# Kernel optimization log

Measured on AMD Instinct MI355X. Metric: run time of the kernel, lower is better.

## Reference

```python
import jax, jax.numpy as jnp
import numpy as np

D, H, FFN_D, B, LT, LS = 1024, 16, 4096, 4, 1024, 1024
EPS = 1e-5  # torch LayerNorm default
NEG = -10000000000.0


def setup_inputs() -> dict:
    key = jax.random.key(0)
    ks = iter(jax.random.split(key, 64))
    s = 0.02
    n = lambda shape: jax.random.normal(next(ks), shape, jnp.float32) * s
    inp = {
        'enc_output': n((LS, B, D)),
        'embedded': n((LT, B, D)),
        'src_mask': jnp.zeros((LS, B), jnp.bool_),
        'tgt_mask': jnp.zeros((LT, B), jnp.bool_),
    }
    for p in ('mmha', 'ed'):
        for w in ('q', 'k', 'v', 'o'):
            inp[f'{p}_w{w}'] = n((D, D))
            inp[f'{p}_b{w}'] = jnp.zeros((D,), jnp.float32)
    inp['ffn_w1'] = n((FFN_D, D)); inp['ffn_b1'] = jnp.zeros((FFN_D,), jnp.float32)
    inp['ffn_w2'] = n((D, FFN_D)); inp['ffn_b2'] = jnp.zeros((D,), jnp.float32)
    for i in range(3):
        inp[f'ln{i}_g'] = jnp.ones((D,), jnp.float32)
        inp[f'ln{i}_b'] = jnp.zeros((D,), jnp.float32)
    return inp


def _ln(x, g, b):
    m = x.mean(-1, keepdims=True)
    v = ((x - m) ** 2).mean(-1, keepdims=True)
    return (x - m) / jnp.sqrt(v + EPS) * g + b


def _mha(qx, kx, vx, wq, bq, wk, bk, wv, bv, wo, bo, mask):
    # qx: (Lq,B,D); kx,vx: (Lk,B,D); mask broadcastable to (B,H,Lq,Lk), True=masked
    Lq, Bn, Dm = qx.shape
    dk = Dm // H
    proj = lambda x, w, bb: (x @ w.T + bb).reshape(x.shape[0], Bn, H, dk).transpose(1, 2, 0, 3)
    q, k, v = proj(qx, wq, bq), proj(kx, wk, bk), proj(vx, wv, bv)  # (B,H,L,dk)
    scores = jnp.einsum('bhqd,bhkd->bhqk', q, k) / np.float32(np.sqrt(dk))
    scores = jnp.where(mask, NEG, scores)  # masked_fill semantics
    w = jax.nn.softmax(scores, axis=-1)  # dropout is identity in eval
    attn = jnp.einsum('bhqk,bhkd->bhqd', w, v).transpose(2, 0, 1, 3).reshape(Lq, Bn, Dm)
    return attn @ wo.T + bo


def reference(enc_output, embedded, src_mask, tgt_mask,
              mmha_wq, mmha_bq, mmha_wk, mmha_bk, mmha_wv, mmha_bv, mmha_wo, mmha_bo,
              ed_wq, ed_bq, ed_wk, ed_bk, ed_wv, ed_bv, ed_wo, ed_bo,
              ffn_w1, ffn_b1, ffn_w2, ffn_b2,
              ln0_g, ln0_b, ln1_g, ln1_b, ln2_g, ln2_b):
    Lt = embedded.shape[0]
    causal = jnp.triu(jnp.ones((Lt, Lt), jnp.bool_), 1)[None, None]      # (1,1,Lt,Lt)
    tmask = tgt_mask.T[:, None, None, :]                                  # (B,1,1,Lt)
    # Sublayer 0: masked self-attention (computed but UNUSED downstream,
    # faithfully mirroring the original forward which discards self_attn).
    self_attn = embedded + _mha(_ln(embedded, ln0_g, ln0_b), _ln(embedded, ln0_g, ln0_b), _ln(embedded, ln0_g, ln0_b),
                                mmha_wq, mmha_bq, mmha_wk, mmha_bk, mmha_wv, mmha_bv, mmha_wo, mmha_bo,
                                causal | tmask)
    del self_attn
    # Sublayer 1: enc-dec attention; residual input is `embedded` (as in source).
    smask = src_mask.T[:, None, None, :]                                  # (B,1,1,Ls)
    q_in = _ln(embedded, ln1_g, ln1_b)
    enc_dec = embedded + _mha(q_in, enc_output, enc_output,
                              ed_wq, ed_bq, ed_wk, ed_bk, ed_wv, ed_bv, ed_wo, ed_bo,
                              smask)
    # Sublayer 2: FFN
    z = _ln(enc_dec, ln2_g, ln2_b)
    ffn = jnp.maximum(z @ ffn_w1.T + ffn_b1, 0.0) @ ffn_w2.T + ffn_b2
    return enc_dec + ffn
```

## Files before the change

### kernel.cpp

```cpp
#include <hip/hip_runtime.h>
#include <cstdint>
#include <math.h>

constexpr int NH  = 16;
constexpr int DKH = 64;
constexpr int SEQ = 1024;
constexpr int NB  = 4;
constexpr int DM  = 1024;
constexpr int DF  = 4096;

typedef __bf16 bf16;
typedef __bf16 bf16x4 __attribute__((ext_vector_type(4)));
typedef __bf16 bf16x8 __attribute__((ext_vector_type(8)));
typedef float  f32x4  __attribute__((ext_vector_type(4)));

#define MFMA16(a, b, c) __builtin_amdgcn_mfma_f32_16x16x32_bf16((a), (b), (c), 0, 0, 0)

__device__ __forceinline__ void gload_lds16(const void* g, void* l) {
  __builtin_amdgcn_global_load_lds(
      (const __attribute__((address_space(1))) unsigned int*)(uintptr_t)g,
      (__attribute__((address_space(3))) unsigned int*)(uintptr_t)l,
      16, 0, 0);
}

template <int BK>
__device__ __forceinline__ int swz(int row) {
  return (BK == 32) ? ((row >> 1) & 3) : (row & 7);
}

template <int ROWS, int BK>
__device__ __forceinline__ void stage_tile(const bf16* __restrict__ g, int ldg,
                                           bf16* __restrict__ l, int t) {
  constexpr int ITER = ROWS * BK / 2048;
#pragma unroll
  for (int i = 0; i < ITER; ++i) {
    const int off = (i * 256 + t) * 8;
    const int row = off / BK;
    const int cc = (off & (BK - 1)) >> 3;
    const int sc = cc ^ swz<BK>(row);
    gload_lds16(&g[(size_t)row * ldg + (sc << 3)], &l[off]);
  }
}

__global__ __launch_bounds__(256) void cast4_kernel(const float* __restrict__ i0, const float* __restrict__ i1,
                                                    const float* __restrict__ i2, const float* __restrict__ i3,
                                                    bf16* __restrict__ o0, bf16* __restrict__ o1,
                                                    bf16* __restrict__ o2, bf16* __restrict__ o3) {
  const int sel = blockIdx.x >> 10;
  const int idx = (blockIdx.x & 1023) * 256 + threadIdx.x;
  const float* in = sel == 0 ? i0 : sel == 1 ? i1 : sel == 2 ? i2 : i3;
  bf16* out = sel == 0 ? o0 : sel == 1 ? o1 : sel == 2 ? o2 : o3;
  const float4 v = ((const float4*)in)[idx];
  bf16x4 ov;
  ov[0] = (bf16)v.x; ov[1] = (bf16)v.y; ov[2] = (bf16)v.z; ov[3] = (bf16)v.w;
  ((bf16x4*)out)[idx] = ov;
}

__global__ __launch_bounds__(256) void cast3_kernel(const float* __restrict__ i0, const float* __restrict__ i1,
                                                    const float* __restrict__ i2,
                                                    bf16* __restrict__ o0, bf16* __restrict__ o1,
                                                    bf16* __restrict__ o2) {
  const int sel = blockIdx.x >> 12;
  const int idx = (blockIdx.x & 4095) * 256 + threadIdx.x;
  const float* in = sel == 0 ? i0 : sel == 1 ? i1 : i2;
  bf16* out = sel == 0 ? o0 : sel == 1 ? o1 : o2;
  const float4 v = ((const float4*)in)[idx];
  bf16x4 ov;
  ov[0] = (bf16)v.x; ov[1] = (bf16)v.y; ov[2] = (bf16)v.z; ov[3] = (bf16)v.w;
  ((bf16x4*)out)[idx] = ov;
}

__global__ __launch_bounds__(256) void ln_kernel(const float* __restrict__ x,
                                                 const float* __restrict__ gam,
                                                 const float* __restrict__ bet,
                                                 bf16* __restrict__ out) {
  const int row = blockIdx.x, t = threadIdx.x;
  const float4 v = ((const float4*)(x + (size_t)row * DM))[t];
  float s  = v.x + v.y + v.z + v.w;
  float s2 = v.x * v.x + v.y * v.y + v.z * v.z + v.w * v.w;
#pragma unroll
  for (int m = 1; m < 64; m <<= 1) { s += __shfl_xor(s, m); s2 += __shfl_xor(s2, m); }
  __shared__ float red[8];
  const int w = t >> 6;
  if ((t & 63) == 0) { red[w] = s; red[4 + w] = s2; }
  __syncthreads();
  s  = red[0] + red[1] + red[2] + red[3];
  s2 = red[4] + red[5] + red[6] + red[7];
  const float mean = s * (1.f / DM);
  const float var  = s2 * (1.f / DM) - mean * mean;
  const float rstd = rsqrtf(var + 1e-5f);
  const float4 g4 = ((const float4*)gam)[t];
  const float4 b4 = ((const float4*)bet)[t];
  bf16x4 ov;
  ov[0] = (bf16)((v.x - mean) * rstd * g4.x + b4.x);
  ov[1] = (bf16)((v.y - mean) * rstd * g4.y + b4.y);
  ov[2] = (bf16)((v.z - mean) * rstd * g4.z + b4.z);
  ov[3] = (bf16)((v.w - mean) * rstd * g4.w + b4.w);
  ((bf16x4*)(out + (size_t)row * DM))[t] = ov;
}

enum { EPI_QKV = 0, EPI_O = 3, EPI_F1 = 4, EPI_F2 = 5 };

struct GParams {
  const bf16* A;
  const bf16* A2;
  const bf16* W;
  const float* b0;
  const float* b1;
  const float* b2;
  const float* resid;
  void* out;
  void* out1;
  void* out2;
  int N;
  int K;
};

template <int MODE, int BN, int BK>
__global__ __launch_bounds__(256, 3) void gemm2(GParams p) {
  constexpr int BM = 128;
  constexpr int WTM = (BN == 128) ? 64 : 32;
  constexpr int MI = WTM / 16;
  __shared__ __align__(16) bf16 As[2][BM * BK];
  __shared__ __align__(16) bf16 Bs[2][BN * BK];
  const int t = threadIdx.x, lane = t & 63, w = t >> 6;
  const int lr = lane & 15, lg = lane >> 4;
  const int wr = (BN == 128) ? (w >> 1) : w;
  const int wc = (BN == 128) ? (w & 1) : 0;
  const int m0 = blockIdx.x * BM, n0 = blockIdx.y * BN;
  const bf16* Ap = (MODE == EPI_QKV && n0 >= 1024) ? p.A2 : p.A;
  const f32x4 FZ = {0.f, 0.f, 0.f, 0.f};
  f32x4 acc[MI][4];
#pragma unroll
  for (int i = 0; i < MI; ++i)
#pragma unroll
    for (int j = 0; j < 4; ++j) acc[i][j] = FZ;

  const int nk = p.K / BK;
  stage_tile<BM, BK>(&Ap[(size_t)m0 * p.K], p.K, As[0], t);
  stage_tile<BN, BK>(&p.W[(size_t)n0 * p.K], p.K, Bs[0], t);
  asm volatile("s_waitcnt vmcnt(0)" ::: "memory");
  __syncthreads();

  int cur = 0;
  for (int kt = 0; kt < nk; ++kt) {
    if (kt + 1 < nk) {
      stage_tile<BM, BK>(&Ap[(size_t)m0 * p.K + (size_t)(kt + 1) * BK], p.K, As[cur ^ 1], t);
      stage_tile<BN, BK>(&p.W[(size_t)n0 * p.K + (size_t)(kt + 1) * BK], p.K, Bs[cur ^ 1], t);
    }
    const bf16* Asl = As[cur];
    const bf16* Bsl = Bs[cur];
#pragma unroll
    for (int kh = 0; kh < BK / 32; ++kh) {
      bf16x8 af[MI], bfr[4];
#pragma unroll
      for (int i = 0; i < MI; ++i) {
        const int row = wr * WTM + i * 16 + lr;
        const int c = (kh * 4 + lg) ^ swz<BK>(row);
        af[i] = *(const bf16x8*)&Asl[row * BK + c * 8];
      }
#pragma unroll
      for (int j = 0; j < 4; ++j) {
        const int row = wc * 64 + j * 16 + lr;
        const int c = (kh * 4 + lg) ^ swz<BK>(row);
        bfr[j] = *(const bf16x8*)&Bsl[row * BK + c * 8];
      }
#pragma unroll
      for (int i = 0; i < MI; ++i)
#pragma unroll
        for (int j = 0; j < 4; ++j) acc[i][j] = MFMA16(af[i], bfr[j], acc[i][j]);
    }
    asm volatile("s_waitcnt vmcnt(0)" ::: "memory");
    __syncthreads();
    cur ^= 1;
  }

#pragma unroll
  for (int i = 0; i < MI; ++i) {
#pragma unroll
    for (int j = 0; j < 4; ++j) {
      const int c = n0 + wc * 64 + j * 16 + lr;
      float bj;
      if constexpr (MODE == EPI_QKV)
        bj = (c < 1024 ? p.b0 : c < 2048 ? p.b1 : p.b2)[c & 1023];
      else
        bj = p.b0[c];
#pragma unroll
      for (int g = 0; g < 4; ++g) {
        const int r = m0 + wr * WTM + i * 16 + 4 * lg + g;
        float v = acc[i][j][g] + bj;
        if constexpr (MODE == EPI_QKV) {
          const int cl = c & 1023;
          const size_t sidx = (((size_t)((r & 3) * NH + (cl >> 6)) << 10) + (r >> 2)) * DKH + (cl & 63);
          if (c < 1024)
            ((bf16*)p.out)[sidx] = (bf16)(v * 0.125f);
          else if (c < 2048)
            ((bf16*)p.out1)[sidx] = (bf16)v;
          else
            ((bf16*)p.out2)[(((size_t)((r & 3) * NH + (cl >> 6)) * DKH + (cl & 63)) << 10) + (r >> 2)] = (bf16)v;
        } else if constexpr (MODE == EPI_O) {
          const size_t idx = (size_t)r * p.N + c;
          ((float*)p.out)[idx] = v + p.resid[idx];
        } else if constexpr (MODE == EPI_F1) {
          ((bf16*)p.out)[(size_t)r * p.N + c] = (bf16)fmaxf(v, 0.f);
        } else {
          const size_t idx = (size_t)r * p.N + c;
          ((float*)p.out)[idx] = v + p.resid[idx];
        }
      }
    }
  }
}

__global__ __launch_bounds__(512, 4) void attn_kernel(const bf16* __restrict__ Qg,
                                                      const bf16* __restrict__ Kg,
                                                      const bf16* __restrict__ Vtg,
                                                      const unsigned char* __restrict__ smask,
                                                      bf16* __restrict__ Og) {
  __shared__ __align__(16) bf16 Ks[2][4096];
  __shared__ __align__(16) bf16 Vs[2][4096];
  __shared__ __align__(16) bf16 Ps[8][1152];
  const int t = threadIdx.x, lane = t & 63, w = t >> 6;
  const int lr = lane & 15, lg = lane >> 4;
  const int id = blockIdx.x;
  const int bh = ((id >> 6) << 3) | (id & 7);
  const int qt = (id >> 3) & 7;
  const int b = bh >> 4, h = bh & 15;
  const int q0 = qt * 128 + w * 16;
  const size_t base = (size_t)bh << 16;

  bf16x8 qa[2];
#pragma unroll
  for (int c = 0; c < 2; ++c)
    qa[c] = *(const bf16x8*)&Qg[base + (size_t)(q0 + lr) * DKH + c * 32 + lg * 8];

  const f32x4 FZ = {0.f, 0.f, 0.f, 0.f};
  f32x4 o[4];
  float mrun[4], lrun[4];
#pragma unroll
  for (int g = 0; g < 4; ++g) { mrun[g] = -INFINITY; lrun[g] = 0.f; o[g] = FZ; }

  {
    const int off = t * 8;
    const int hi = off >> 11, mid = (off >> 5) & 63, lo = off & 31;
    gload_lds16(&Kg[base + (size_t)mid * DKH + hi * 32 + lo], &Ks[0][off]);
    gload_lds16(&Vtg[base + (size_t)mid * SEQ + hi * 32 + lo], &Vs[0][off]);
  }
  asm volatile("s_waitcnt vmcnt(0)" ::: "memory");
  __syncthreads();

  int cur = 0;
  for (int kt = 0; kt < SEQ / 64; ++kt) {
    const int kv0 = kt * 64;
    if (kt + 1 < SEQ / 64) {
      const int off = t * 8;
      const int hi = off >> 11, mid = (off >> 5) & 63, lo = off & 31;
      gload_lds16(&Kg[base + (size_t)(kv0 + 64 + mid) * DKH + hi * 32 + lo], &Ks[cur ^ 1][off]);
      gload_lds16(&Vtg[base + (size_t)mid * SEQ + kv0 + 64 + hi * 32 + lo], &Vs[cur ^ 1][off]);
    }

    f32x4 s[4];
#pragma unroll
    for (int n = 0; n < 4; ++n) s[n] = FZ;
#pragma unroll
    for (int c = 0; c < 2; ++c) {
      bf16x8 kb[4];
#pragma unroll
      for (int n = 0; n < 4; ++n)
        kb[n] = *(const bf16x8*)&Ks[cur][c * 2048 + (n * 16 + lr) * 32 + lg * 8];
      __builtin_amdgcn_s_setprio(1);
#pragma unroll
      for (int n = 0; n < 4; ++n) s[n] = MFMA16(qa[c], kb[n], s[n]);
      __builtin_amdgcn_s_setprio(0);
    }

    float madd[4];
#pragma unroll
    for (int n = 0; n < 4; ++n)
      madd[n] = smask[(size_t)(kv0 + n * 16 + lr) * NB + b] ? -1e10f : 0.f;
#pragma unroll
    for (int n = 0; n < 4; ++n)
#pragma unroll
      for (int g = 0; g < 4; ++g) s[n][g] += madd[n];

#pragma unroll
    for (int g = 0; g < 4; ++g) {
      float tm = fmaxf(fmaxf(s[0][g], s[1][g]), fmaxf(s[2][g], s[3][g]));
      tm = fmaxf(tm, __shfl_xor(tm, 1));
      tm = fmaxf(tm, __shfl_xor(tm, 2));
      tm = fmaxf(tm, __shfl_xor(tm, 4));
      tm = fmaxf(tm, __shfl_xor(tm, 8));
      const float mnew = fmaxf(mrun[g], tm);
      float ts = 0.f;
#pragma unroll
      for (int n = 0; n < 4; ++n) {
        const float p = __expf(s[n][g] - mnew);
        s[n][g] = p;
        ts += p;
      }
      ts += __shfl_xor(ts, 1);
      ts += __shfl_xor(ts, 2);
      ts += __shfl_xor(ts, 4);
      ts += __shfl_xor(ts, 8);
      const float sc = __expf(mrun[g] - mnew);
      lrun[g] = lrun[g] * sc + ts;
      mrun[g] = mnew;
#pragma unroll
      for (int n = 0; n < 4; ++n) o[n][g] *= sc;
    }

    bf16* Pw = &Ps[w][0];
#pragma unroll
    for (int n = 0; n < 4; ++n)
#pragma unroll
      for (int g = 0; g < 4; ++g)
        Pw[(4 * lg + g) * 72 + n * 16 + lr] = (bf16)s[n][g];
    __builtin_amdgcn_sched_barrier(0);

#pragma unroll
    for (int c = 0; c < 2; ++c) {
      const bf16x8 pa = *(const bf16x8*)&Pw[lr * 72 + c * 32 + lg * 8];
      bf16x8 vb[4];
#pragma unroll
      for (int n = 0; n < 4; ++n)
        vb[n] = *(const bf16x8*)&Vs[cur][c * 2048 + (n * 16 + lr) * 32 + lg * 8];
      __builtin_amdgcn_s_setprio(1);
#pragma unroll
      for (int n = 0; n < 4; ++n) o[n] = MFMA16(pa, vb[n], o[n]);
      __builtin_amdgcn_s_setprio(0);
    }

    asm volatile("s_waitcnt vmcnt(0)" ::: "memory");
    __syncthreads();
    cur ^= 1;
  }

#pragma unroll
  for (int g = 0; g < 4; ++g) {
    const int l = q0 + 4 * lg + g;
    const float inv = 1.0f / lrun[g];
#pragma unroll
    for (int n = 0; n < 4; ++n)
      Og[(size_t)(l * NB + b) * DM + h * 64 + n * 16 + lr] = (bf16)(o[n][g] * inv);
  }
}

extern "C" void kernel_launch(void* const* d_in, const int* in_sizes, int n_in,
                              void* d_out, int out_size, void* d_ws, size_t ws_size,
                              hipStream_t stream) {
  const float* enc = (const float*)d_in[0];
  const float* emb = (const float*)d_in[1];
  const unsigned char* smask = (const unsigned char*)d_in[2];
  const float* wq = (const float*)d_in[12]; const float* bq = (const float*)d_in[13];
  const float* wk = (const float*)d_in[14]; const float* bk = (const float*)d_in[15];
  const float* wv = (const float*)d_in[16]; const float* bv = (const float*)d_in[17];
  const float* wo = (const float*)d_in[18]; const float* bo = (const float*)d_in[19];
  const float* w1 = (const float*)d_in[20]; const float* b1 = (const float*)d_in[21];
  const float* w2 = (const float*)d_in[22]; const float* b2 = (const float*)d_in[23];
  const float* g1 = (const float*)d_in[26]; const float* be1 = (const float*)d_in[27];
  const float* g2 = (const float*)d_in[28]; const float* be2 = (const float*)d_in[29];

  char* ws = (char*)d_ws;
  const size_t MB = (size_t)1 << 20;
  bf16* wqkv_bf = (bf16*)(ws + 0 * MB);
  bf16* wo_bf   = (bf16*)(ws + 6 * MB);
  bf16* w1_bf   = (bf16*)(ws + 8 * MB);
  bf16* w2_bf   = (bf16*)(ws + 16 * MB);
  bf16* enc_bf  = (bf16*)(ws + 24 * MB);
  bf16* z_bf    = enc_bf;
  bf16* qin_bf  = (bf16*)(ws + 32 * MB);
  bf16* attn_bf = qin_bf;
  bf16* Q_bf    = (bf16*)(ws + 40 * MB);
  bf16* K_bf    = (bf16*)(ws + 48 * MB);
  bf16* Vt_bf   = (bf16*)(ws + 56 * MB);
  float* encdec = (float*)(ws + 64 * MB);
  bf16* h_bf    = (bf16*)(ws + 80 * MB);

  cast4_kernel<<<4096, 256, 0, stream>>>(wq, wk, wv, wo,
                                         wqkv_bf, wqkv_bf + (1 << 20), wqkv_bf + (2 << 20), wo_bf);
  cast3_kernel<<<12288, 256, 0, stream>>>(w1, w2, enc, w1_bf, w2_bf, enc_bf);

  ln_kernel<<<4096, 256, 0, stream>>>(emb, g1, be1, qin_bf);

  {
    GParams p{qin_bf, enc_bf, wqkv_bf, bq, bk, bv, nullptr, Q_bf, K_bf, Vt_bf, 3072, DM};
    gemm2<EPI_QKV, 128, 32><<<dim3(32, 24), 256, 0, stream>>>(p);
  }

  attn_kernel<<<512, 512, 0, stream>>>(Q_bf, K_bf, Vt_bf, smask, attn_bf);

  {
    GParams p{attn_bf, nullptr, wo_bf, bo, nullptr, nullptr, emb, encdec, nullptr, nullptr, DM, DM};
    gemm2<EPI_O, 64, 64><<<dim3(32, 16), 256, 0, stream>>>(p);
  }

  ln_kernel<<<4096, 256, 0, stream>>>(encdec, g2, be2, z_bf);

  {
    GParams p{z_bf, nullptr, w1_bf, b1, nullptr, nullptr, nullptr, h_bf, nullptr, nullptr, DF, DM};
    gemm2<EPI_F1, 128, 32><<<dim3(32, 32), 256, 0, stream>>>(p);
  }
  {
    GParams p{h_bf, nullptr, w2_bf, b2, nullptr, nullptr, encdec, d_out, nullptr, nullptr, DM, DF};
    gemm2<EPI_F2, 64, 64><<<dim3(32, 16), 256, 0, stream>>>(p);
  }
}
```

Baseline: 388.3 us.

## Fuse prep casts with first LayerNorm; swizzle attention LDS; lazy softmax rescale

Merges the two weight/encoder cast kernels and the first LayerNorm into one prep kernel, removing two launches and their tail gaps. In the attention kernel, K and V tiles are stored in LDS with an XOR swizzle on the 16-byte chunk index so the MFMA operand reads hit fewer bank conflicts. The online softmax now rescales the running max and output only when some row's new max exceeds the old one by more than 8, which skips exp and multiply work on most tiles. The lazy rescale allows unnormalized exponentials up to e^8, which is fine in fp32 but slightly changes the bf16 rounding of P.

```diff
diff --git a/kernel.cpp b/kernel.cpp
--- a/kernel.cpp
+++ b/kernel.cpp
@@ -42,32 +42,60 @@
   }
 }
 
-__global__ __launch_bounds__(256) void cast4_kernel(const float* __restrict__ i0, const float* __restrict__ i1,
-                                                    const float* __restrict__ i2, const float* __restrict__ i3,
-                                                    bf16* __restrict__ o0, bf16* __restrict__ o1,
-                                                    bf16* __restrict__ o2, bf16* __restrict__ o3) {
-  const int sel = blockIdx.x >> 10;
-  const int idx = (blockIdx.x & 1023) * 256 + threadIdx.x;
-  const float* in = sel == 0 ? i0 : sel == 1 ? i1 : sel == 2 ? i2 : i3;
-  bf16* out = sel == 0 ? o0 : sel == 1 ? o1 : sel == 2 ? o2 : o3;
-  const float4 v = ((const float4*)in)[idx];
+__global__ __launch_bounds__(256) void prep_kernel(
+    const float* __restrict__ wq, const float* __restrict__ wk,
+    const float* __restrict__ wv, const float* __restrict__ wo,
+    const float* __restrict__ w1, const float* __restrict__ w2,
+    const float* __restrict__ enc, const float* __restrict__ emb,
+    const float* __restrict__ g1, const float* __restrict__ be1,
+    bf16* __restrict__ wqkv_bf, bf16* __restrict__ wo_bf,
+    bf16* __restrict__ w1_bf, bf16* __restrict__ w2_bf,
+    bf16* __restrict__ enc_bf, bf16* __restrict__ qin_bf) {
+  const int bid = blockIdx.x, t = threadIdx.x;
+  if (bid < 16384) {
+    const float* in;
+    bf16* out;
+    int idx;
+    if (bid < 4096) {
+      const int sel = bid >> 10;
+      in = sel == 0 ? wq : sel == 1 ? wk : sel == 2 ? wv : wo;
+      out = sel == 3 ? wo_bf : wqkv_bf + ((size_t)sel << 20);
+      idx = (bid & 1023) * 256 + t;
+    } else {
+      const int sel = (bid - 4096) >> 12;
+      in = sel == 0 ? w1 : sel == 1 ? w2 : enc;
+      out = sel == 0 ? w1_bf : sel == 1 ? w2_bf : enc_bf;
+      idx = ((bid - 4096) & 4095) * 256 + t;
+    }
+    const float4 v = ((const float4*)in)[idx];
+    bf16x4 ov;
+    ov[0] = (bf16)v.x; ov[1] = (bf16)v.y; ov[2] = (bf16)v.z; ov[3] = (bf16)v.w;
+    ((bf16x4*)out)[idx] = ov;
+    return;
+  }
+  const int row = bid - 16384;
+  const float4 v = ((const float4*)(emb + (size_t)row * DM))[t];
+  float s  = v.x + v.y + v.z + v.w;
+  float s2 = v.x * v.x + v.y * v.y + v.z * v.z + v.w * v.w;
+#pragma unroll
+  for (int m = 1; m < 64; m <<= 1) { s += __shfl_xor(s, m); s2 += __shfl_xor(s2, m); }
+  __shared__ float red[8];
+  const int w = t >> 6;
+  if ((t & 63) == 0) { red[w] = s; red[4 + w] = s2; }
+  __syncthreads();
+  s  = red[0] + red[1] + red[2] + red[3];
+  s2 = red[4] + red[5] + red[6] + red[7];
+  const float mean = s * (1.f / DM);
+  const float var  = s2 * (1.f / DM) - mean * mean;
+  const float rstd = rsqrtf(var + 1e-5f);
+  const float4 g4 = ((const float4*)g1)[t];
+  const float4 b4 = ((const float4*)be1)[t];
   bf16x4 ov;
-  ov[0] = (bf16)v.x; ov[1] = (bf16)v.y; ov[2] = (bf16)v.z; ov[3] = (bf16)v.w;
-  ((bf16x4*)out)[idx] = ov;
-}
-
-__global__ __launch_bounds__(256) void cast3_kernel(const float* __restrict__ i0, const float* __restrict__ i1,
-                                                    const float* __restrict__ i2,
-                                                    bf16* __restrict__ o0, bf16* __restrict__ o1,
-                                                    bf16* __restrict__ o2) {
-  const int sel = blockIdx.x >> 12;
-  const int idx = (blockIdx.x & 4095) * 256 + threadIdx.x;
-  const float* in = sel == 0 ? i0 : sel == 1 ? i1 : i2;
-  bf16* out = sel == 0 ? o0 : sel == 1 ? o1 : o2;
-  const float4 v = ((const float4*)in)[idx];
-  bf16x4 ov;
-  ov[0] = (bf16)v.x; ov[1] = (bf16)v.y; ov[2] = (bf16)v.z; ov[3] = (bf16)v.w;
-  ((bf16x4*)out)[idx] = ov;
+  ov[0] = (bf16)((v.x - mean) * rstd * g4.x + b4.x);
+  ov[1] = (bf16)((v.y - mean) * rstd * g4.y + b4.y);
+  ov[2] = (bf16)((v.z - mean) * rstd * g4.z + b4.z);
+  ov[3] = (bf16)((v.w - mean) * rstd * g4.w + b4.w);
+  ((bf16x4*)(qin_bf + (size_t)row * DM))[t] = ov;
 }
 
 __global__ __launch_bounds__(256) void ln_kernel(const float* __restrict__ x,
@@ -240,23 +268,23 @@
 #pragma unroll
   for (int g = 0; g < 4; ++g) { mrun[g] = -INFINITY; lrun[g] = 0.f; o[g] = FZ; }
 
-  {
-    const int off = t * 8;
-    const int hi = off >> 11, mid = (off >> 5) & 63, lo = off & 31;
-    gload_lds16(&Kg[base + (size_t)mid * DKH + hi * 32 + lo], &Ks[0][off]);
-    gload_lds16(&Vtg[base + (size_t)mid * SEQ + hi * 32 + lo], &Vs[0][off]);
-  }
+  const int soff = t * 8;
+  const int shi = soff >> 11, smid = (soff >> 5) & 63;
+  const int ssc = (((soff >> 3) & 3) ^ ((smid >> 1) & 3)) << 3;
+
+  gload_lds16(&Kg[base + (size_t)smid * DKH + shi * 32 + ssc], &Ks[0][soff]);
+  gload_lds16(&Vtg[base + (size_t)smid * SEQ + shi * 32 + ssc], &Vs[0][soff]);
   asm volatile("s_waitcnt vmcnt(0)" ::: "memory");
   __syncthreads();
+
+  const int rsw = ((lr >> 1) & 3);
 
   int cur = 0;
   for (int kt = 0; kt < SEQ / 64; ++kt) {
     const int kv0 = kt * 64;
     if (kt + 1 < SEQ / 64) {
-      const int off = t * 8;
-      const int hi = off >> 11, mid = (off >> 5) & 63, lo = off & 31;
-      gload_lds16(&Kg[base + (size_t)(kv0 + 64 + mid) * DKH + hi * 32 + lo], &Ks[cur ^ 1][off]);
-      gload_lds16(&Vtg[base + (size_t)mid * SEQ + kv0 + 64 + hi * 32 + lo], &Vs[cur ^ 1][off]);
+      gload_lds16(&Kg[base + (size_t)(kv0 + 64 + smid) * DKH + shi * 32 + ssc], &Ks[cur ^ 1][soff]);
+      gload_lds16(&Vtg[base + (size_t)smid * SEQ + kv0 + 64 + shi * 32 + ssc], &Vs[cur ^ 1][soff]);
     }
 
     f32x4 s[4];
@@ -267,7 +295,7 @@
       bf16x8 kb[4];
 #pragma unroll
       for (int n = 0; n < 4; ++n)
-        kb[n] = *(const bf16x8*)&Ks[cur][c * 2048 + (n * 16 + lr) * 32 + lg * 8];
+        kb[n] = *(const bf16x8*)&Ks[cur][c * 2048 + (n * 16 + lr) * 32 + ((lg ^ rsw) << 3)];
       __builtin_amdgcn_s_setprio(1);
 #pragma unroll
       for (int n = 0; n < 4; ++n) s[n] = MFMA16(qa[c], kb[n], s[n]);
@@ -283,6 +311,8 @@
 #pragma unroll
       for (int g = 0; g < 4; ++g) s[n][g] += madd[n];
 
+    float tm4[4];
+    bool needany = false;
 #pragma unroll
     for (int g = 0; g < 4; ++g) {
       float tm = fmaxf(fmaxf(s[0][g], s[1][g]), fmaxf(s[2][g], s[3][g]));
@@ -290,11 +320,26 @@
       tm = fmaxf(tm, __shfl_xor(tm, 2));
       tm = fmaxf(tm, __shfl_xor(tm, 4));
       tm = fmaxf(tm, __shfl_xor(tm, 8));
-      const float mnew = fmaxf(mrun[g], tm);
+      tm4[g] = tm;
+      needany |= (tm > mrun[g] + 8.f);
+    }
+    if (__any(needany)) {
+#pragma unroll
+      for (int g = 0; g < 4; ++g) {
+        const float mnew = fmaxf(mrun[g], tm4[g]);
+        const float sc = __expf(mrun[g] - mnew);
+        mrun[g] = mnew;
+        lrun[g] *= sc;
+#pragma unroll
+        for (int n = 0; n < 4; ++n) o[n][g] *= sc;
+      }
+    }
+#pragma unroll
+    for (int g = 0; g < 4; ++g) {
       float ts = 0.f;
 #pragma unroll
       for (int n = 0; n < 4; ++n) {
-        const float p = __expf(s[n][g] - mnew);
+        const float p = __expf(s[n][g] - mrun[g]);
         s[n][g] = p;
         ts += p;
       }
@@ -302,11 +347,7 @@
       ts += __shfl_xor(ts, 2);
       ts += __shfl_xor(ts, 4);
       ts += __shfl_xor(ts, 8);
-      const float sc = __expf(mrun[g] - mnew);
-      lrun[g] = lrun[g] * sc + ts;
-      mrun[g] = mnew;
-#pragma unroll
-      for (int n = 0; n < 4; ++n) o[n][g] *= sc;
+      lrun[g] += ts;
     }
 
     bf16* Pw = &Ps[w][0];
@@ -323,7 +364,7 @@
       bf16x8 vb[4];
 #pragma unroll
       for (int n = 0; n < 4; ++n)
-        vb[n] = *(const bf16x8*)&Vs[cur][c * 2048 + (n * 16 + lr) * 32 + lg * 8];
+        vb[n] = *(const bf16x8*)&Vs[cur][c * 2048 + (n * 16 + lr) * 32 + ((lg ^ rsw) << 3)];
       __builtin_amdgcn_s_setprio(1);
 #pragma unroll
       for (int n = 0; n < 4; ++n) o[n] = MFMA16(pa, vb[n], o[n]);
@@ -376,11 +417,8 @@
   float* encdec = (float*)(ws + 64 * MB);
   bf16* h_bf    = (bf16*)(ws + 80 * MB);
 
-  cast4_kernel<<<4096, 256, 0, stream>>>(wq, wk, wv, wo,
-                                         wqkv_bf, wqkv_bf + (1 << 20), wqkv_bf + (2 << 20), wo_bf);
-  cast3_kernel<<<12288, 256, 0, stream>>>(w1, w2, enc, w1_bf, w2_bf, enc_bf);
-
-  ln_kernel<<<4096, 256, 0, stream>>>(emb, g1, be1, qin_bf);
+  prep_kernel<<<20480, 256, 0, stream>>>(wq, wk, wv, wo, w1, w2, enc, emb, g1, be1,
+                                         wqkv_bf, wo_bf, w1_bf, w2_bf, enc_bf, qin_bf);
 
   {
     GParams p{qin_bf, enc_bf, wqkv_bf, bq, bk, bv, nullptr, Q_bf, K_bf, Vt_bf, 3072, DM};
```

Result: no change. 394.9 us (+1.7%).
